# Kernel optimization log

Measured on AMD Instinct MI355X. Metric: run time of the kernel, lower is better.

Reference implementation:

```python
import jax, jax.numpy as jnp
import numpy as np

N_POL = 20000; N_COMP = 80000; N = N_POL + N_COMP
E = 1000000; EMB = 128; HID = 256; HEADS = 8; OUT = 128; EA = 5
NEG_SLOPE = 0.2; LN_EPS = 1e-5


def setup_inputs() -> dict:
    ks = jax.random.split(jax.random.key(0), 24)
    def rn(i, shape, s=0.1):
        return jax.random.normal(ks[i], shape, jnp.float32) * s
    C1 = HID // HEADS  # per-head channels of conv1
    return dict(
        pol_feat=rn(0, (N_POL, 7), 1.0),
        state_ids=jax.random.randint(ks[1], (N_POL,), 0, 55),
        comp_cat=jax.random.randint(ks[2], (N_COMP, 2), 0, 16),
        comp_price=rn(3, (N_COMP, 1), 1.0),
        edge_index=jax.random.randint(ks[4], (2, E), 0, N),
        edge_attr=rn(5, (E, EA), 1.0),
        Wp=rn(6, (7, EMB)), bp=jnp.zeros((EMB,), jnp.float32),
        state_emb=rn(7, (55, EMB)), sector_emb=rn(8, (16, 8)), industry_emb=rn(9, (150, 8)),
        Wc=rn(10, (17, EMB)), bc=jnp.zeros((EMB,), jnp.float32),
        ln_g=jnp.ones((EMB,), jnp.float32), ln_b=jnp.zeros((EMB,), jnp.float32),
        W1=rn(11, (EMB, HEADS * C1)), att_src1=rn(12, (HEADS, C1)), att_dst1=rn(13, (HEADS, C1)),
        We1=rn(14, (EA, HEADS * C1)), att_e1=rn(15, (HEADS, C1)), b1=jnp.zeros((HID,), jnp.float32),
        W2=rn(16, (HID, OUT)), att_src2=rn(17, (1, OUT)), att_dst2=rn(18, (1, OUT)),
        We2=rn(19, (EA, OUT)), att_e2=rn(20, (1, OUT)), b2=jnp.zeros((OUT,), jnp.float32),
    )


def _add_self_loops(src, dst, ea, n):
    # PyG add_self_loops with fill_value='mean': self-loop edge_attr = mean of
    # incoming edge attrs per dst node (0 for isolated nodes).
    loop = jnp.arange(n, dtype=src.dtype)
    cnt = jax.ops.segment_sum(jnp.ones(dst.shape, jnp.float32), dst, num_segments=n)
    loop_attr = jax.ops.segment_sum(ea, dst, num_segments=n) / jnp.maximum(cnt, 1.0)[:, None]
    return (jnp.concatenate([src, loop]), jnp.concatenate([dst, loop]),
            jnp.concatenate([ea, loop_attr], 0))


def _gat(x, src, dst, ea, W, a_src, a_dst, We, a_e, bias, concat):
    # PyG GATConv (shared lin for src/dst, edge_dim attention, eval mode).
    n = x.shape[0]
    H, C = a_src.shape
    xw = (x @ W).reshape(n, H, C)                 # [n,H,C]
    al_s = jnp.sum(xw * a_src, -1)                # [n,H]
    al_d = jnp.sum(xw * a_dst, -1)                # [n,H]
    ew = (ea @ We).reshape(-1, H, C)              # [Etot,H,C]
    al_e = jnp.sum(ew * a_e, -1)                  # [Etot,H]
    alpha = jax.nn.leaky_relu(al_s[src] + al_d[dst] + al_e, NEG_SLOPE)
    amax = jax.ops.segment_max(alpha, dst, num_segments=n)
    ex = jnp.exp(alpha - amax[dst])
    denom = jax.ops.segment_sum(ex, dst, num_segments=n)
    alpha = ex / (denom[dst] + 1e-16)             # segment softmax over dst
    out = jax.ops.segment_sum(xw[src] * alpha[:, :, None], dst, num_segments=n)
    out = out.reshape(n, H * C) if concat else out.mean(1)
    return out + bias


def reference(pol_feat, state_ids, comp_cat, comp_price, edge_index, edge_attr,
              Wp, bp, state_emb, sector_emb, industry_emb, Wc, bc, ln_g, ln_b,
              W1, att_src1, att_dst1, We1, att_e1, b1,
              W2, att_src2, att_dst2, We2, att_e2, b2):
    pol = jax.nn.relu(pol_feat @ Wp + bp) + state_emb[state_ids]
    comp_in = jnp.concatenate([sector_emb[comp_cat[:, 0]], industry_emb[comp_cat[:, 1]], comp_price], 1)
    comp = jax.nn.relu(comp_in @ Wc + bc)
    x = jnp.concatenate([pol, comp], 0)           # [N,EMB]
    mu = jnp.mean(x, -1, keepdims=True)
    var = jnp.var(x, -1, keepdims=True)
    x = (x - mu) / jnp.sqrt(var + LN_EPS) * ln_g + ln_b
    src, dst, ea = _add_self_loops(edge_index[0], edge_index[1], edge_attr, x.shape[0])
    h = jax.nn.elu(_gat(x, src, dst, ea, W1, att_src1, att_dst1, We1, att_e1, b1, True))
    return _gat(h, src, dst, ea, W2, att_src2, att_dst2, We2, att_e2, b2, False)
```

## Files before the change

kernel.cpp:

```cpp
#include <hip/hip_runtime.h>
#include <hip/hip_fp16.h>
#include <math.h>

#define N_POL 20000
#define N_COMP 80000
#define NN (N_POL + N_COMP)
#define EE 1000000
#define NB1 ((NN + 1023) / 1024)
#define LOG2E 1.44269504f

typedef short bf16x8 __attribute__((ext_vector_type(8)));
typedef float f32x4 __attribute__((ext_vector_type(4)));

struct __align__(16) PEdge {
  int s;
  float ale2;
  unsigned short a1[8];
  unsigned pad[2];
};

__device__ __forceinline__ float wave_sum(float v) {
#pragma unroll
  for (int o = 32; o > 0; o >>= 1) v += __shfl_xor(v, o);
  return v;
}
__device__ __forceinline__ float wave_max(float v) {
#pragma unroll
  for (int o = 32; o > 0; o >>= 1) v = fmaxf(v, __shfl_xor(v, o));
  return v;
}
__device__ __forceinline__ unsigned short f2bf(float f) {
  unsigned b = __float_as_uint(f);
  return (unsigned short)((b + 0x7FFFu + ((b >> 16) & 1u)) >> 16);
}
__device__ __forceinline__ float bf2f(unsigned short u) {
  return __uint_as_float(((unsigned)u) << 16);
}
__device__ __forceinline__ unsigned short f2h(float f) {
  __half h = __float2half_rn(f);
  return *(unsigned short*)&h;
}
__device__ __forceinline__ float h2f(unsigned short u) {
  __half h = *(__half*)&u;
  return __half2float(h);
}

__global__ __launch_bounds__(256) void k_prep(
    const float* W1, const float* W2, const float* as2, const float* ad2,
    const float* We1, const float* ae1, const float* We2, const float* ae2,
    const float* sector_emb, const float* industry_emb, const float* Wc,
    unsigned short* W1t, unsigned short* W2t, float* Ts, float* Ti, float* us2,
    float* ud2, float* V1, float* V2) {
  int id = blockIdx.x * 256 + threadIdx.x;
  if (id < 32768) {
    int n = id >> 7, k = id & 127;
    W1t[id] = f2bf(W1[k * 256 + n]);
  } else if (id < 65536) {
    int id2 = id - 32768;
    int n = id2 >> 8, k = id2 & 255;
    W2t[id2] = f2bf(W2[k * 128 + n]);
  } else if (id < 67584) {
    int id2 = id - 65536;
    int n = id2 >> 7, c = id2 & 127;
    float a = 0.f;
#pragma unroll
    for (int k = 0; k < 8; k++) a = fmaf(sector_emb[n * 8 + k], Wc[k * 128 + c], a);
    Ts[id2] = a;
  } else if (id < 86784) {
    int id2 = id - 67584;
    int n = id2 >> 7, c = id2 & 127;
    float a = 0.f;
#pragma unroll
    for (int k = 0; k < 8; k++) a = fmaf(industry_emb[n * 8 + k], Wc[(8 + k) * 128 + c], a);
    Ti[id2] = a;
  } else if (id < 87040) {
    int t = id - 86784;
    float s = 0.f, d = 0.f;
    for (int c = 0; c < 128; c++) {
      float w = W2[t * 128 + c];
      s = fmaf(w, as2[c], s);
      d = fmaf(w, ad2[c], d);
    }
    us2[t] = s * LOG2E;
    ud2[t] = d * LOG2E;
  } else if (id < 87104) {
    int t = id - 87040;
    int k = t >> 3, h = t & 7;
    if (k < 5) {
      float v = 0.f;
      for (int c = 0; c < 32; c++) v = fmaf(We1[k * 256 + h * 32 + c], ae1[h * 32 + c], v);
      V1[k * 8 + h] = v * LOG2E;
    }
  } else if (id < 87109) {
    int t = id - 87104;
    float v = 0.f;
    for (int c = 0; c < 128; c++) v = fmaf(We2[t * 128 + c], ae2[c], v);
    V2[t] = v * LOG2E;
  }
}

__global__ __launch_bounds__(256) void k_encode(
    const float* pol_feat, const int* state_ids, const int* comp_cat,
    const float* comp_price, const float* Wp, const float* bp, const float* state_emb,
    const float* Ts, const float* Ti, const float* Wc, const float* bc,
    const float* ln_g, const float* ln_b, unsigned short* x) {
  int t = threadIdx.x;
  int i = blockIdx.x * 2 + (t >> 7), c = t & 127;
  float v;
  if (i < N_POL) {
    float acc = bp[c];
#pragma unroll
    for (int k = 0; k < 7; k++) acc = fmaf(pol_feat[i * 7 + k], Wp[k * 128 + c], acc);
    v = fmaxf(acc, 0.f) + state_emb[state_ids[i] * 128 + c];
  } else {
    int j = i - N_POL;
    int sc = comp_cat[2 * j], in = comp_cat[2 * j + 1];
    float acc = Ts[sc * 128 + c] + Ti[in * 128 + c] +
                comp_price[j] * Wc[16 * 128 + c] + bc[c];
    v = fmaxf(acc, 0.f);
  }
  __shared__ float red[4];
  int wid = t >> 6, lane = t & 63;
  int base = (t >> 7) << 1;
  float s = wave_sum(v);
  if (lane == 0) red[wid] = s;
  __syncthreads();
  float mu = (red[base] + red[base + 1]) * (1.f / 128.f);
  float t0 = v - mu;
  __syncthreads();
  float s2 = wave_sum(t0 * t0);
  if (lane == 0) red[wid] = s2;
  __syncthreads();
  float var = (red[base] + red[base + 1]) * (1.f / 128.f);
  float r = rsqrtf(var + 1e-5f);
  float xf = t0 * r * ln_g[c] + ln_b[c];
  x[(size_t)i * 128 + c] = f2bf(xf);
}

__global__ void k_hist(const int* dst, unsigned* hist) {
  int e = blockIdx.x * blockDim.x + threadIdx.x;
  if (e < EE) atomicAdd(&hist[dst[e]], 1u);
}
__global__ __launch_bounds__(1024) void k_scan1(const unsigned* hist, unsigned* rowptr,
                                                unsigned* part) {
  __shared__ unsigned sc[1024];
  int t = threadIdx.x;
  int i = blockIdx.x * 1024 + t;
  unsigned v = (i < NN) ? hist[i] : 0u;
  sc[t] = v;
  __syncthreads();
  for (int o = 1; o < 1024; o <<= 1) {
    unsigned add = (t >= o) ? sc[t - o] : 0u;
    __syncthreads();
    sc[t] += add;
    __syncthreads();
  }
  if (i < NN) rowptr[i] = sc[t] - v;
  if (t == 1023) part[blockIdx.x] = sc[1023];
}
__global__ __launch_bounds__(128) void k_scan2(unsigned* part) {
  __shared__ unsigned sc[128];
  int t = threadIdx.x;
  unsigned v = (t < NB1) ? part[t] : 0u;
  sc[t] = v;
  __syncthreads();
  for (int o = 1; o < 128; o <<= 1) {
    unsigned add = (t >= o) ? sc[t - o] : 0u;
    __syncthreads();
    sc[t] += add;
    __syncthreads();
  }
  if (t < NB1) part[t] = sc[t] - v;
}
__global__ void k_scan3(unsigned* rowptr, const unsigned* part, unsigned* cursor) {
  int i = blockIdx.x * blockDim.x + threadIdx.x;
  if (i < NN) {
    unsigned r = rowptr[i] + part[i >> 10];
    rowptr[i] = r;
    cursor[i] = r;
  }
  if (i == 0) rowptr[NN] = EE;
}
__global__ void k_scatter(const int* src, const int* dst, const float* ea,
                          const float* V1, const float* V2, unsigned* cursor,
                          PEdge* ep) {
  int e = blockIdx.x * blockDim.x + threadIdx.x;
  if (e >= EE) return;
  int d = dst[e];
  unsigned pos = atomicAdd(&cursor[d], 1u);
  float av[5];
#pragma unroll
  for (int k = 0; k < 5; k++) av[k] = ea[(size_t)e * 5 + k];
  float a2 = 0.f;
#pragma unroll
  for (int k = 0; k < 5; k++) a2 = fmaf(av[k], V2[k], a2);
  unsigned short hb[8];
#pragma unroll
  for (int hh = 0; hh < 8; hh++) {
    float a1 = 0.f;
#pragma unroll
    for (int k = 0; k < 5; k++) a1 = fmaf(av[k], V1[k * 8 + hh], a1);
    hb[hh] = f2h(a1);
  }
  uint4 w0, w1;
  w0.x = (unsigned)src[e];
  w0.y = __float_as_uint(a2);
  w0.z = (unsigned)hb[0] | ((unsigned)hb[1] << 16);
  w0.w = (unsigned)hb[2] | ((unsigned)hb[3] << 16);
  w1.x = (unsigned)hb[4] | ((unsigned)hb[5] << 16);
  w1.y = (unsigned)hb[6] | ((unsigned)hb[7] << 16);
  w1.z = 0u; w1.w = 0u;
  uint4* p = (uint4*)(ep + pos);
  p[0] = w0;
  p[1] = w1;
}

__global__ __launch_bounds__(256) void k_gemm1(const unsigned short* x,
                                               const unsigned short* W1t,
                                               unsigned short* xw1) {
  __shared__ char wlds[65536];
  int tid = threadIdx.x;
#pragma unroll
  for (int it = 0; it < 16; it++) {
    int cch = it * 256 + tid;
    int row = cch >> 4, seg = cch & 15;
    uint4 v = *(const uint4*)(W1t + row * 128 + seg * 8);
    *(uint4*)(&wlds[(row * 256 + seg * 16) ^ ((row & 7) << 4)]) = v;
  }
  __syncthreads();
  int wid = tid >> 6, l = tid & 63;
  int cl = l & 15, kh = l >> 4;
  int swz = (cl & 7) << 4;
  long r0 = (long)blockIdx.x * 128 + wid * 32;
  f32x4 acc[2][16];
#pragma unroll
  for (int rt = 0; rt < 2; rt++)
#pragma unroll
    for (int nt = 0; nt < 16; nt++) acc[rt][nt] = {0.f, 0.f, 0.f, 0.f};
  long ra0 = r0 + cl; if (ra0 > NN - 1) ra0 = NN - 1;
  long ra1 = r0 + 16 + cl; if (ra1 > NN - 1) ra1 = NN - 1;
#pragma unroll
  for (int kk = 0; kk < 4; kk++) {
    bf16x8 a0 = *(const bf16x8*)(x + ra0 * 128 + kk * 32 + kh * 8);
    bf16x8 a1 = *(const bf16x8*)(x + ra1 * 128 + kk * 32 + kh * 8);
#pragma unroll
    for (int nt = 0; nt < 16; nt++) {
      bf16x8 b = *(const bf16x8*)(&wlds[(((nt * 16 + cl) * 256) + kk * 64 + kh * 16) ^ swz]);
      acc[0][nt] = __builtin_amdgcn_mfma_f32_16x16x32_bf16(a0, b, acc[0][nt], 0, 0, 0);
      acc[1][nt] = __builtin_amdgcn_mfma_f32_16x16x32_bf16(a1, b, acc[1][nt], 0, 0, 0);
    }
  }
#pragma unroll
  for (int rt = 0; rt < 2; rt++)
#pragma unroll
    for (int nt = 0; nt < 16; nt++)
#pragma unroll
      for (int j = 0; j < 4; j++) {
        long row = r0 + rt * 16 + kh * 4 + j;
        if (row < NN) xw1[row * 256 + nt * 16 + cl] = f2bf(acc[rt][nt][j]);
      }
}

__global__ __launch_bounds__(256) void k_al(const unsigned short* xw1, const float* as1,
                                            const float* ad1, float* al_s1,
                                            float* al_d1) {
  int w = threadIdx.x >> 6, lane = threadIdx.x & 63;
  int i = blockIdx.x * 4 + w;
  if (i >= NN) return;
  ushort4 xv = ((const ushort4*)(xw1 + (size_t)i * 256))[lane];
  float4 as = ((const float4*)as1)[lane];
  float4 ad = ((const float4*)ad1)[lane];
  float x0 = bf2f(xv.x), x1 = bf2f(xv.y), x2 = bf2f(xv.z), x3 = bf2f(xv.w);
  float s = x0 * as.x + x1 * as.y + x2 * as.z + x3 * as.w;
  float d = x0 * ad.x + x1 * ad.y + x2 * ad.z + x3 * ad.w;
#pragma unroll
  for (int o = 1; o < 8; o <<= 1) {
    s += __shfl_xor(s, o);
    d += __shfl_xor(d, o);
  }
  if ((lane & 7) == 0) {
    al_s1[i * 8 + (lane >> 3)] = s * LOG2E;
    al_d1[i * 8 + (lane >> 3)] = d * LOG2E;
  }
}

__global__ __launch_bounds__(256) void k_gemm2(const unsigned short* h,
                                               const unsigned short* W2t,
                                               unsigned short* xw2) {
  __shared__ char wlds[65536];
  int tid = threadIdx.x;
#pragma unroll
  for (int it = 0; it < 16; it++) {
    int cch = it * 256 + tid;
    int row = cch >> 5, seg = cch & 31;
    uint4 v = *(const uint4*)(W2t + row * 256 + seg * 8);
    *(uint4*)(&wlds[(row * 512 + seg * 16) ^ ((row & 7) << 4)]) = v;
  }
  __syncthreads();
  int wid = tid >> 6, l = tid & 63;
  int cl = l & 15, kh = l >> 4;
  int swz = (cl & 7) << 4;
  long r0 = (long)blockIdx.x * 128 + wid * 32;
  f32x4 acc[2][8];
#pragma unroll
  for (int rt = 0; rt < 2; rt++)
#pragma unroll
    for (int nt = 0; nt < 8; nt++) acc[rt][nt] = {0.f, 0.f, 0.f, 0.f};
  long ra0 = r0 + cl; if (ra0 > NN - 1) ra0 = NN - 1;
  long ra1 = r0 + 16 + cl; if (ra1 > NN - 1) ra1 = NN - 1;
#pragma unroll
  for (int kk = 0; kk < 8; kk++) {
    bf16x8 a0 = *(const bf16x8*)(h + ra0 * 256 + kk * 32 + kh * 8);
    bf16x8 a1 = *(const bf16x8*)(h + ra1 * 256 + kk * 32 + kh * 8);
#pragma unroll
    for (int nt = 0; nt < 8; nt++) {
      bf16x8 b = *(const bf16x8*)(&wlds[(((nt * 16 + cl) * 512) + kk * 64 + kh * 16) ^ swz]);
      acc[0][nt] = __builtin_amdgcn_mfma_f32_16x16x32_bf16(a0, b, acc[0][nt], 0, 0, 0);
      acc[1][nt] = __builtin_amdgcn_mfma_f32_16x16x32_bf16(a1, b, acc[1][nt], 0, 0, 0);
    }
  }
#pragma unroll
  for (int rt = 0; rt < 2; rt++)
#pragma unroll
    for (int nt = 0; nt < 8; nt++)
#pragma unroll
      for (int j = 0; j < 4; j++) {
        long row = r0 + rt * 16 + kh * 4 + j;
        if (row < NN) xw2[row * 128 + nt * 16 + cl] = f2bf(acc[rt][nt][j]);
      }
}

__global__ __launch_bounds__(256) void k_gat1(
    const unsigned* rowptr, const PEdge* ep, const float* al_s1, const float* al_d1,
    const unsigned short* xw1, const float* b1, const float* us2, const float* ud2,
    unsigned short* h, float* al_s2, float* al_d2) {
  int w = threadIdx.x >> 6, lane = threadIdx.x & 63;
  int i = blockIdx.x * 4 + w;
  if (i >= NN) return;
  int r0 = rowptr[i], r1 = rowptr[i + 1];
  int hh = lane & 7;
  int js = lane >> 3;
  int ah = lane >> 3;
  float ald = al_d1[i * 8 + hh];
  float m = -1e30f, l = 0.f;
  float a0 = 0.f, a1 = 0.f, a2 = 0.f, a3 = 0.f;
  float alesum = 0.f;

  auto chunk16 = [&](int jb) {
    int jc0 = jb + js, jc1 = jb + 8 + js;
    int s0 = *(const int*)&ep[jc0];
    int s1 = *(const int*)&ep[jc1];
    float e0 = h2f(((const unsigned short*)&ep[jc0])[4 + hh]);
    float e1 = h2f(((const unsigned short*)&ep[jc1])[4 + hh]);
    alesum += e0 + e1;
    float g0 = al_s1[s0 * 8 + hh] + ald + e0;
    g0 = g0 > 0.f ? g0 : 0.2f * g0;
    float g1 = al_s1[s1 * 8 + hh] + ald + e1;
    g1 = g1 > 0.f ? g1 : 0.2f * g1;
    float cm = fmaxf(g0, g1);
    cm = fmaxf(cm, __shfl_xor(cm, 8));
    cm = fmaxf(cm, __shfl_xor(cm, 16));
    cm = fmaxf(cm, __shfl_xor(cm, 32));
    float mn = fmaxf(m, cm);
    float sc = exp2f(m - mn);
    float p0 = exp2f(g0 - mn), p1 = exp2f(g1 - mn);
    float ps = p0 + p1;
    ps += __shfl_xor(ps, 8);
    ps += __shfl_xor(ps, 16);
    ps += __shfl_xor(ps, 32);
    l = l * sc + ps;
    m = mn;
    float asc = __shfl(sc, ah);
    a0 *= asc; a1 *= asc; a2 *= asc; a3 *= asc;
#pragma unroll
    for (int jj = 0; jj < 8; jj++) {
      float pj = __shfl(p0, jj * 8 + ah);
      int sj = __shfl(s0, jj * 8);
      ushort4 xv = ((const ushort4*)(xw1 + (size_t)sj * 256))[lane];
      a0 = fmaf(pj, bf2f(xv.x), a0);
      a1 = fmaf(pj, bf2f(xv.y), a1);
      a2 = fmaf(pj, bf2f(xv.z), a2);
      a3 = fmaf(pj, bf2f(xv.w), a3);
    }
#pragma unroll
    for (int jj = 0; jj < 8; jj++) {
      float pj = __shfl(p1, jj * 8 + ah);
      int sj = __shfl(s1, jj * 8);
      ushort4 xv = ((const ushort4*)(xw1 + (size_t)sj * 256))[lane];
      a0 = fmaf(pj, bf2f(xv.x), a0);
      a1 = fmaf(pj, bf2f(xv.y), a1);
      a2 = fmaf(pj, bf2f(xv.z), a2);
      a3 = fmaf(pj, bf2f(xv.w), a3);
    }
  };

  auto chunk8 = [&](int jb, int cnt) {
    bool valid = js < cnt;
    int jc = jb + (valid ? js : cnt - 1);
    int s = *(const int*)&ep[jc];
    float ale = h2f(((const unsigned short*)&ep[jc])[4 + hh]);
    if (!valid) ale = 0.f;
    alesum += ale;
    float logit = -1e30f;
    if (valid) {
      float al = al_s1[s * 8 + hh] + ald + ale;
      logit = al > 0.f ? al : 0.2f * al;
    }
    float cm = logit;
    cm = fmaxf(cm, __shfl_xor(cm, 8));
    cm = fmaxf(cm, __shfl_xor(cm, 16));
    cm = fmaxf(cm, __shfl_xor(cm, 32));
    float mn = fmaxf(m, cm);
    float sc = exp2f(m - mn);
    float p = exp2f(logit - mn);
    float ps = p;
    ps += __shfl_xor(ps, 8);
    ps += __shfl_xor(ps, 16);
    ps += __shfl_xor(ps, 32);
    l = l * sc + ps;
    m = mn;
    float asc = __shfl(sc, ah);
    a0 *= asc; a1 *= asc; a2 *= asc; a3 *= asc;
    for (int jj = 0; jj < cnt; jj++) {
      float pj = __shfl(p, jj * 8 + ah);
      int sj = __shfl(s, jj * 8);
      ushort4 xv = ((const ushort4*)(xw1 + (size_t)sj * 256))[lane];
      a0 = fmaf(pj, bf2f(xv.x), a0);
      a1 = fmaf(pj, bf2f(xv.y), a1);
      a2 = fmaf(pj, bf2f(xv.z), a2);
      a3 = fmaf(pj, bf2f(xv.w), a3);
    }
  };

  int jb = r0;
  for (; jb + 16 <= r1; jb += 16) chunk16(jb);
  if (jb + 8 <= r1) { chunk8(jb, 8); jb += 8; }
  if (jb < r1) chunk8(jb, r1 - jb);

  alesum += __shfl_xor(alesum, 8);
  alesum += __shfl_xor(alesum, 16);
  alesum += __shfl_xor(alesum, 32);
  float inv = 1.f / fmaxf((float)(r1 - r0), 1.f);
  float aleS = alesum * inv;
  {
    float al = al_s1[i * 8 + hh] + ald + aleS;
    float logit = al > 0.f ? al : 0.2f * al;
    float mn = fmaxf(m, logit);
    float sc = exp2f(m - mn);
    float p = exp2f(logit - mn);
    l = l * sc + p;
    m = mn;
    float asc = __shfl(sc, ah);
    float pj = __shfl(p, ah);
    ushort4 xv = ((const ushort4*)(xw1 + (size_t)i * 256))[lane];
    a0 = fmaf(pj, bf2f(xv.x), a0 * asc);
    a1 = fmaf(pj, bf2f(xv.y), a1 * asc);
    a2 = fmaf(pj, bf2f(xv.z), a2 * asc);
    a3 = fmaf(pj, bf2f(xv.w), a3 * asc);
  }
  float lh = __shfl(l, ah);
  float invl = 1.f / (lh + 1e-16f);
  float4 bv = ((const float4*)b1)[lane];
  float v0 = a0 * invl + bv.x, v1 = a1 * invl + bv.y;
  float v2 = a2 * invl + bv.z, v3 = a3 * invl + bv.w;
  v0 = v0 > 0.f ? v0 : expm1f(v0);
  v1 = v1 > 0.f ? v1 : expm1f(v1);
  v2 = v2 > 0.f ? v2 : expm1f(v2);
  v3 = v3 > 0.f ? v3 : expm1f(v3);
  ushort4 hv;
  hv.x = f2bf(v0); hv.y = f2bf(v1); hv.z = f2bf(v2); hv.w = f2bf(v3);
  ((ushort4*)(h + (size_t)i * 256))[lane] = hv;
  float4 uv = ((const float4*)us2)[lane];
  float4 dv = ((const float4*)ud2)[lane];
  float ps2 = v0 * uv.x + v1 * uv.y + v2 * uv.z + v3 * uv.w;
  float pd2 = v0 * dv.x + v1 * dv.y + v2 * dv.z + v3 * dv.w;
  ps2 = wave_sum(ps2);
  pd2 = wave_sum(pd2);
  if (lane == 0) { al_s2[i] = ps2; al_d2[i] = pd2; }
}

__global__ __launch_bounds__(256) void k_gat2(
    const unsigned* rowptr, const PEdge* ep, const float* al_s2, const float* al_d2,
    const unsigned short* xw2, const float* b2, float* out) {
  int w = threadIdx.x >> 6, lane = threadIdx.x & 63;
  int i = blockIdx.x * 4 + w;
  if (i >= NN) return;
  int r0 = rowptr[i], r1 = rowptr[i + 1];
  float ald = al_d2[i];
  float m = -1e30f, l = 0.f, a0 = 0.f, a1 = 0.f;
  float alesum = 0.f;

  auto chunk = [&](int jb, int cnt) {
    bool valid = lane < cnt;
    int jc = jb + (valid ? lane : cnt - 1);
    int2 sv = *(const int2*)&ep[jc];
    int s = sv.x;
    float ale = valid ? __uint_as_float((unsigned)sv.y) : 0.f;
    alesum += ale;
    float logit = -1e30f;
    if (valid) {
      float al = al_s2[s] + ald + ale;
      logit = al > 0.f ? al : 0.2f * al;
    }
    float cm = wave_max(logit);
    float mn = fmaxf(m, cm);
    float sc = exp2f(m - mn);
    float p = exp2f(logit - mn);
    float ps = wave_sum(p);
    l = l * sc + ps;
    m = mn;
    a0 *= sc; a1 *= sc;
    for (int jj = 0; jj < cnt; jj++) {
      float pj = __shfl(p, jj);
      int sj = __shfl(s, jj);
      ushort2 xv = ((const ushort2*)(xw2 + (size_t)sj * 128))[lane];
      a0 = fmaf(pj, bf2f(xv.x), a0);
      a1 = fmaf(pj, bf2f(xv.y), a1);
    }
  };
  int jb = r0;
  for (; jb + 64 <= r1; jb += 64) chunk(jb, 64);
  if (jb < r1) chunk(jb, r1 - jb);

  alesum = wave_sum(alesum);
  float inv = 1.f / fmaxf((float)(r1 - r0), 1.f);
  float aleS = alesum * inv;
  {
    float al = al_s2[i] + ald + aleS;
    float logit = al > 0.f ? al : 0.2f * al;
    float mn = fmaxf(m, logit);
    float sc = exp2f(m - mn);
    float p = exp2f(logit - mn);
    l = l * sc + p;
    ushort2 xv = ((const ushort2*)(xw2 + (size_t)i * 128))[lane];
    a0 = fmaf(p, bf2f(xv.x), a0 * sc);
    a1 = fmaf(p, bf2f(xv.y), a1 * sc);
  }
  float invl = 1.f / (l + 1e-16f);
  float2 bv = ((const float2*)b2)[lane];
  float2 ov = {a0 * invl + bv.x, a1 * invl + bv.y};
  ((float2*)(out + (size_t)i * 128))[lane] = ov;
}

extern "C" void kernel_launch(void* const* d_in, const int* in_sizes, int n_in,
                              void* d_out, int out_size, void* d_ws, size_t ws_size,
                              hipStream_t stream) {
  const float* pol_feat = (const float*)d_in[0];
  const int* state_ids = (const int*)d_in[1];
  const int* comp_cat = (const int*)d_in[2];
  const float* comp_price = (const float*)d_in[3];
  const int* edge_index = (const int*)d_in[4];
  const float* edge_attr = (const float*)d_in[5];
  const float* Wp = (const float*)d_in[6];
  const float* bp = (const float*)d_in[7];
  const float* state_emb = (const float*)d_in[8];
  const float* sector_emb = (const float*)d_in[9];
  const float* industry_emb = (const float*)d_in[10];
  const float* Wc = (const float*)d_in[11];
  const float* bc = (const float*)d_in[12];
  const float* ln_g = (const float*)d_in[13];
  const float* ln_b = (const float*)d_in[14];
  const float* W1 = (const float*)d_in[15];
  const float* as1 = (const float*)d_in[16];
  const float* ad1 = (const float*)d_in[17];
  const float* We1 = (const float*)d_in[18];
  const float* ae1 = (const float*)d_in[19];
  const float* b1 = (const float*)d_in[20];
  const float* W2 = (const float*)d_in[21];
  const float* as2 = (const float*)d_in[22];
  const float* ad2 = (const float*)d_in[23];
  const float* We2 = (const float*)d_in[24];
  const float* ae2 = (const float*)d_in[25];
  const float* b2 = (const float*)d_in[26];
  const int* srcv = edge_index;
  const int* dstv = edge_index + EE;
  float* out = (float*)d_out;

  size_t off = 0;
  auto alloc = [&](size_t nbytes) -> char* {
    char* p = (char*)d_ws + off;
    off += ((nbytes + 255) & ~(size_t)255);
    return p;
  };
  char* regA = alloc((size_t)NN * 512);
  char* regB = alloc((size_t)NN * 512);
  unsigned short* xw1 = (unsigned short*)regA;
  unsigned short* xw2 = (unsigned short*)regA;
  unsigned short* h = (unsigned short*)regB;
  unsigned short* x = (unsigned short*)regB;
  float* al_s1 = (float*)alloc((size_t)NN * 8 * 4);
  float* al_d1 = (float*)alloc((size_t)NN * 8 * 4);
  float* al_s2 = (float*)alloc((size_t)NN * 4);
  float* al_d2 = (float*)alloc((size_t)NN * 4);
  float* us2 = (float*)alloc(256 * 4);
  float* ud2 = (float*)alloc(256 * 4);
  float* V1 = (float*)alloc(64 * 4);
  float* V2 = (float*)alloc(8 * 4);
  float* Ts = (float*)alloc(16 * 128 * 4);
  float* Ti = (float*)alloc(150 * 128 * 4);
  unsigned short* W1t = (unsigned short*)alloc(32768 * 2);
  unsigned short* W2t = (unsigned short*)alloc(32768 * 2);
  unsigned* hist = (unsigned*)alloc((size_t)NN * 4);
  unsigned* rowptr = (unsigned*)alloc((size_t)(NN + 1) * 4);
  unsigned* cursor = (unsigned*)alloc((size_t)NN * 4);
  unsigned* part = (unsigned*)alloc((size_t)NB1 * 4);
  PEdge* ep = (PEdge*)alloc((size_t)EE * sizeof(PEdge));

  hipMemsetAsync(hist, 0, (size_t)NN * 4, stream);

  k_prep<<<341, 256, 0, stream>>>(W1, W2, as2, ad2, We1, ae1, We2, ae2, sector_emb,
                                  industry_emb, Wc, W1t, W2t, Ts, Ti, us2, ud2, V1, V2);
  k_encode<<<NN / 2, 256, 0, stream>>>(pol_feat, state_ids, comp_cat, comp_price, Wp,
                                       bp, state_emb, Ts, Ti, Wc, bc, ln_g, ln_b, x);
  k_hist<<<(EE + 255) / 256, 256, 0, stream>>>(dstv, hist);
  k_scan1<<<NB1, 1024, 0, stream>>>(hist, rowptr, part);
  k_scan2<<<1, 128, 0, stream>>>(part);
  k_scan3<<<(NN + 255) / 256, 256, 0, stream>>>(rowptr, part, cursor);
  k_scatter<<<(EE + 255) / 256, 256, 0, stream>>>(srcv, dstv, edge_attr, V1, V2,
                                                  cursor, ep);
  k_gemm1<<<(NN + 127) / 128, 256, 0, stream>>>(x, W1t, xw1);
  k_al<<<NN / 4, 256, 0, stream>>>(xw1, as1, ad1, al_s1, al_d1);
  k_gat1<<<NN / 4, 256, 0, stream>>>(rowptr, ep, al_s1, al_d1, xw1, b1, us2, ud2, h,
                                     al_s2, al_d2);
  k_gemm2<<<(NN + 127) / 128, 256, 0, stream>>>(h, W2t, xw2);
  k_gat2<<<NN / 4, 256, 0, stream>>>(rowptr, ep, al_s2, al_d2, xw2, b2, out);
}
```

Measured before the change: 420.9 us.

## Shrink edge records to raw fp16 attrs, fuse attention logits into gemm1

Each edge record shrinks from 32 to 16 bytes. It now holds the source index and the five raw edge attributes in fp16, and the per-head edge logits are recomputed inside the GAT kernels from V1/V2. The attention-source/destination dot products move into the gemm1 epilogue via lane shuffles, which removes the separate k_al pass over xw1. The scan2 kernel is folded into scan3, so every block redoes the 128-entry prefix, and gat2 gains a fully populated 64-edge chunk path. The aim is less memory traffic and fewer launches, paid for with more ALU work per edge and a small change in fp16 rounding of the edge logits.

```diff
diff --git a/kernel.cpp b/kernel.cpp
--- a/kernel.cpp
+++ b/kernel.cpp
@@ -12,12 +12,6 @@
 typedef short bf16x8 __attribute__((ext_vector_type(8)));
 typedef float f32x4 __attribute__((ext_vector_type(4)));
 
-struct __align__(16) PEdge {
-  int s;
-  float ale2;
-  unsigned short a1[8];
-  unsigned pad[2];
-};
 
 __device__ __forceinline__ float wave_sum(float v) {
 #pragma unroll
@@ -40,9 +34,9 @@
   __half h = __float2half_rn(f);
   return *(unsigned short*)&h;
 }
-__device__ __forceinline__ float h2f(unsigned short u) {
-  __half h = *(__half*)&u;
-  return __half2float(h);
+__device__ __forceinline__ float2 h2f2(unsigned u) {
+  __half2 h = *(__half2*)&u;
+  return __half22float2(h);
 }
 
 __global__ __launch_bounds__(256) void k_prep(
@@ -158,32 +152,35 @@
   if (i < NN) rowptr[i] = sc[t] - v;
   if (t == 1023) part[blockIdx.x] = sc[1023];
 }
-__global__ __launch_bounds__(128) void k_scan2(unsigned* part) {
-  __shared__ unsigned sc[128];
+__global__ __launch_bounds__(256) void k_scan3(unsigned* rowptr, const unsigned* part,
+                                               unsigned* cursor) {
+  __shared__ unsigned pref[128];
   int t = threadIdx.x;
-  unsigned v = (t < NB1) ? part[t] : 0u;
-  sc[t] = v;
+  unsigned orig = 0u;
+  if (t < 128) {
+    orig = (t < NB1) ? part[t] : 0u;
+    pref[t] = orig;
+  }
   __syncthreads();
   for (int o = 1; o < 128; o <<= 1) {
-    unsigned add = (t >= o) ? sc[t - o] : 0u;
+    unsigned add = 0u;
+    if (t < 128 && t >= o) add = pref[t - o];
     __syncthreads();
-    sc[t] += add;
+    if (t < 128) pref[t] += add;
     __syncthreads();
   }
-  if (t < NB1) part[t] = sc[t] - v;
-}
-__global__ void k_scan3(unsigned* rowptr, const unsigned* part, unsigned* cursor) {
-  int i = blockIdx.x * blockDim.x + threadIdx.x;
+  if (t < 128) pref[t] -= orig;
+  __syncthreads();
+  int i = blockIdx.x * 256 + t;
   if (i < NN) {
-    unsigned r = rowptr[i] + part[i >> 10];
+    unsigned r = rowptr[i] + pref[i >> 10];
     rowptr[i] = r;
     cursor[i] = r;
   }
   if (i == 0) rowptr[NN] = EE;
 }
 __global__ void k_scatter(const int* src, const int* dst, const float* ea,
-                          const float* V1, const float* V2, unsigned* cursor,
-                          PEdge* ep) {
+                          unsigned* cursor, uint4* ep) {
   int e = blockIdx.x * blockDim.x + threadIdx.x;
   if (e >= EE) return;
   int d = dst[e];
@@ -191,33 +188,19 @@
   float av[5];
 #pragma unroll
   for (int k = 0; k < 5; k++) av[k] = ea[(size_t)e * 5 + k];
-  float a2 = 0.f;
-#pragma unroll
-  for (int k = 0; k < 5; k++) a2 = fmaf(av[k], V2[k], a2);
-  unsigned short hb[8];
-#pragma unroll
-  for (int hh = 0; hh < 8; hh++) {
-    float a1 = 0.f;
-#pragma unroll
-    for (int k = 0; k < 5; k++) a1 = fmaf(av[k], V1[k * 8 + hh], a1);
-    hb[hh] = f2h(a1);
-  }
-  uint4 w0, w1;
-  w0.x = (unsigned)src[e];
-  w0.y = __float_as_uint(a2);
-  w0.z = (unsigned)hb[0] | ((unsigned)hb[1] << 16);
-  w0.w = (unsigned)hb[2] | ((unsigned)hb[3] << 16);
-  w1.x = (unsigned)hb[4] | ((unsigned)hb[5] << 16);
-  w1.y = (unsigned)hb[6] | ((unsigned)hb[7] << 16);
-  w1.z = 0u; w1.w = 0u;
-  uint4* p = (uint4*)(ep + pos);
-  p[0] = w0;
-  p[1] = w1;
+  uint4 w;
+  w.x = (unsigned)src[e];
+  w.y = (unsigned)f2h(av[0]) | ((unsigned)f2h(av[1]) << 16);
+  w.z = (unsigned)f2h(av[2]) | ((unsigned)f2h(av[3]) << 16);
+  w.w = (unsigned)f2h(av[4]);
+  ep[pos] = w;
 }
 
 __global__ __launch_bounds__(256) void k_gemm1(const unsigned short* x,
                                                const unsigned short* W1t,
-                                               unsigned short* xw1) {
+                                               const float* as1, const float* ad1,
+                                               unsigned short* xw1, float* al_s1,
+                                               float* al_d1) {
   __shared__ char wlds[65536];
   int tid = threadIdx.x;
 #pragma unroll
@@ -250,38 +233,38 @@
       acc[1][nt] = __builtin_amdgcn_mfma_f32_16x16x32_bf16(a1, b, acc[1][nt], 0, 0, 0);
     }
   }
+  float as1s[16], ad1s[16];
+#pragma unroll
+  for (int nt = 0; nt < 16; nt++) {
+    as1s[nt] = as1[nt * 16 + cl];
+    ad1s[nt] = ad1[nt * 16 + cl];
+  }
 #pragma unroll
   for (int rt = 0; rt < 2; rt++)
 #pragma unroll
-    for (int nt = 0; nt < 16; nt++)
-#pragma unroll
-      for (int j = 0; j < 4; j++) {
-        long row = r0 + rt * 16 + kh * 4 + j;
-        if (row < NN) xw1[row * 256 + nt * 16 + cl] = f2bf(acc[rt][nt][j]);
+    for (int j = 0; j < 4; j++) {
+      long row = r0 + rt * 16 + kh * 4 + j;
+      bool ok = row < NN;
+#pragma unroll
+      for (int hh = 0; hh < 8; hh++) {
+        float a0 = acc[rt][2 * hh][j];
+        float a1 = acc[rt][2 * hh + 1][j];
+        if (ok) {
+          xw1[row * 256 + (2 * hh) * 16 + cl] = f2bf(a0);
+          xw1[row * 256 + (2 * hh + 1) * 16 + cl] = f2bf(a1);
+        }
+        float sh = a0 * as1s[2 * hh] + a1 * as1s[2 * hh + 1];
+        float dh = a0 * ad1s[2 * hh] + a1 * ad1s[2 * hh + 1];
+        sh += __shfl_xor(sh, 1); sh += __shfl_xor(sh, 2);
+        sh += __shfl_xor(sh, 4); sh += __shfl_xor(sh, 8);
+        dh += __shfl_xor(dh, 1); dh += __shfl_xor(dh, 2);
+        dh += __shfl_xor(dh, 4); dh += __shfl_xor(dh, 8);
+        if (ok && cl == 0) {
+          al_s1[row * 8 + hh] = sh * LOG2E;
+          al_d1[row * 8 + hh] = dh * LOG2E;
+        }
       }
-}
-
-__global__ __launch_bounds__(256) void k_al(const unsigned short* xw1, const float* as1,
-                                            const float* ad1, float* al_s1,
-                                            float* al_d1) {
-  int w = threadIdx.x >> 6, lane = threadIdx.x & 63;
-  int i = blockIdx.x * 4 + w;
-  if (i >= NN) return;
-  ushort4 xv = ((const ushort4*)(xw1 + (size_t)i * 256))[lane];
-  float4 as = ((const float4*)as1)[lane];
-  float4 ad = ((const float4*)ad1)[lane];
-  float x0 = bf2f(xv.x), x1 = bf2f(xv.y), x2 = bf2f(xv.z), x3 = bf2f(xv.w);
-  float s = x0 * as.x + x1 * as.y + x2 * as.z + x3 * as.w;
-  float d = x0 * ad.x + x1 * ad.y + x2 * ad.z + x3 * ad.w;
-#pragma unroll
-  for (int o = 1; o < 8; o <<= 1) {
-    s += __shfl_xor(s, o);
-    d += __shfl_xor(d, o);
-  }
-  if ((lane & 7) == 0) {
-    al_s1[i * 8 + (lane >> 3)] = s * LOG2E;
-    al_d1[i * 8 + (lane >> 3)] = d * LOG2E;
-  }
+    }
 }
 
 __global__ __launch_bounds__(256) void k_gemm2(const unsigned short* h,
@@ -331,9 +314,9 @@
 }
 
 __global__ __launch_bounds__(256) void k_gat1(
-    const unsigned* rowptr, const PEdge* ep, const float* al_s1, const float* al_d1,
-    const unsigned short* xw1, const float* b1, const float* us2, const float* ud2,
-    unsigned short* h, float* al_s2, float* al_d2) {
+    const unsigned* rowptr, const uint4* ep, const float* al_s1, const float* al_d1,
+    const float* V1, const unsigned short* xw1, const float* b1, const float* us2,
+    const float* ud2, unsigned short* h, float* al_s2, float* al_d2) {
   int w = threadIdx.x >> 6, lane = threadIdx.x & 63;
   int i = blockIdx.x * 4 + w;
   if (i >= NN) return;
@@ -341,17 +324,25 @@
   int hh = lane & 7;
   int js = lane >> 3;
   int ah = lane >> 3;
+  float v1k0 = V1[0 * 8 + hh], v1k1 = V1[1 * 8 + hh], v1k2 = V1[2 * 8 + hh];
+  float v1k3 = V1[3 * 8 + hh], v1k4 = V1[4 * 8 + hh];
   float ald = al_d1[i * 8 + hh];
   float m = -1e30f, l = 0.f;
   float a0 = 0.f, a1 = 0.f, a2 = 0.f, a3 = 0.f;
   float alesum = 0.f;
 
+  auto edot = [&](const uint4& rec) {
+    float2 e01 = h2f2(rec.y);
+    float2 e23 = h2f2(rec.z);
+    float e4 = h2f2(rec.w).x;
+    return e01.x * v1k0 + e01.y * v1k1 + e23.x * v1k2 + e23.y * v1k3 + e4 * v1k4;
+  };
+
   auto chunk16 = [&](int jb) {
-    int jc0 = jb + js, jc1 = jb + 8 + js;
-    int s0 = *(const int*)&ep[jc0];
-    int s1 = *(const int*)&ep[jc1];
-    float e0 = h2f(((const unsigned short*)&ep[jc0])[4 + hh]);
-    float e1 = h2f(((const unsigned short*)&ep[jc1])[4 + hh]);
+    uint4 rc0 = ep[jb + js];
+    uint4 rc1 = ep[jb + 8 + js];
+    int s0 = (int)rc0.x, s1 = (int)rc1.x;
+    float e0 = edot(rc0), e1 = edot(rc1);
     alesum += e0 + e1;
     float g0 = al_s1[s0 * 8 + hh] + ald + e0;
     g0 = g0 > 0.f ? g0 : 0.2f * g0;
@@ -397,8 +388,9 @@
   auto chunk8 = [&](int jb, int cnt) {
     bool valid = js < cnt;
     int jc = jb + (valid ? js : cnt - 1);
-    int s = *(const int*)&ep[jc];
-    float ale = h2f(((const unsigned short*)&ep[jc])[4 + hh]);
+    uint4 rc = ep[jc];
+    int s = (int)rc.x;
+    float ale = edot(rc);
     if (!valid) ale = 0.f;
     alesum += ale;
     float logit = -1e30f;
@@ -480,22 +472,56 @@
 }
 
 __global__ __launch_bounds__(256) void k_gat2(
-    const unsigned* rowptr, const PEdge* ep, const float* al_s2, const float* al_d2,
-    const unsigned short* xw2, const float* b2, float* out) {
+    const unsigned* rowptr, const uint4* ep, const float* al_s2, const float* al_d2,
+    const float* V2, const unsigned short* xw2, const float* b2, float* out) {
   int w = threadIdx.x >> 6, lane = threadIdx.x & 63;
   int i = blockIdx.x * 4 + w;
   if (i >= NN) return;
   int r0 = rowptr[i], r1 = rowptr[i + 1];
+  float v2k0 = V2[0], v2k1 = V2[1], v2k2 = V2[2], v2k3 = V2[3], v2k4 = V2[4];
   float ald = al_d2[i];
   float m = -1e30f, l = 0.f, a0 = 0.f, a1 = 0.f;
   float alesum = 0.f;
 
+  auto edot = [&](const uint4& rec) {
+    float2 e01 = h2f2(rec.y);
+    float2 e23 = h2f2(rec.z);
+    float e4 = h2f2(rec.w).x;
+    return e01.x * v2k0 + e01.y * v2k1 + e23.x * v2k2 + e23.y * v2k3 + e4 * v2k4;
+  };
+
+  auto chunkF = [&](int jb) {
+    uint4 rc = ep[jb + lane];
+    int s = (int)rc.x;
+    float ale = edot(rc);
+    alesum += ale;
+    float al = al_s2[s] + ald + ale;
+    float logit = al > 0.f ? al : 0.2f * al;
+    float cm = wave_max(logit);
+    float mn = fmaxf(m, cm);
+    float sc = exp2f(m - mn);
+    float p = exp2f(logit - mn);
+    float ps = wave_sum(p);
+    l = l * sc + ps;
+    m = mn;
+    a0 *= sc; a1 *= sc;
+#pragma unroll 4
+    for (int jj = 0; jj < 64; jj++) {
+      float pj = __shfl(p, jj);
+      int sj = __shfl(s, jj);
+      ushort2 xv = ((const ushort2*)(xw2 + (size_t)sj * 128))[lane];
+      a0 = fmaf(pj, bf2f(xv.x), a0);
+      a1 = fmaf(pj, bf2f(xv.y), a1);
+    }
+  };
+
   auto chunk = [&](int jb, int cnt) {
     bool valid = lane < cnt;
     int jc = jb + (valid ? lane : cnt - 1);
-    int2 sv = *(const int2*)&ep[jc];
-    int s = sv.x;
-    float ale = valid ? __uint_as_float((unsigned)sv.y) : 0.f;
+    uint4 rc = ep[jc];
+    int s = (int)rc.x;
+    float ale = edot(rc);
+    if (!valid) ale = 0.f;
     alesum += ale;
     float logit = -1e30f;
     if (valid) {
@@ -518,8 +544,9 @@
       a1 = fmaf(pj, bf2f(xv.y), a1);
     }
   };
+
   int jb = r0;
-  for (; jb + 64 <= r1; jb += 64) chunk(jb, 64);
+  for (; jb + 64 <= r1; jb += 64) chunkF(jb);
   if (jb < r1) chunk(jb, r1 - jb);
 
   alesum = wave_sum(alesum);
@@ -604,7 +631,7 @@
   unsigned* rowptr = (unsigned*)alloc((size_t)(NN + 1) * 4);
   unsigned* cursor = (unsigned*)alloc((size_t)NN * 4);
   unsigned* part = (unsigned*)alloc((size_t)NB1 * 4);
-  PEdge* ep = (PEdge*)alloc((size_t)EE * sizeof(PEdge));
+  uint4* ep = (uint4*)alloc((size_t)EE * 16);
 
   hipMemsetAsync(hist, 0, (size_t)NN * 4, stream);
 
@@ -614,14 +641,11 @@
                                        bp, state_emb, Ts, Ti, Wc, bc, ln_g, ln_b, x);
   k_hist<<<(EE + 255) / 256, 256, 0, stream>>>(dstv, hist);
   k_scan1<<<NB1, 1024, 0, stream>>>(hist, rowptr, part);
-  k_scan2<<<1, 128, 0, stream>>>(part);
   k_scan3<<<(NN + 255) / 256, 256, 0, stream>>>(rowptr, part, cursor);
-  k_scatter<<<(EE + 255) / 256, 256, 0, stream>>>(srcv, dstv, edge_attr, V1, V2,
-                                                  cursor, ep);
-  k_gemm1<<<(NN + 127) / 128, 256, 0, stream>>>(x, W1t, xw1);
-  k_al<<<NN / 4, 256, 0, stream>>>(xw1, as1, ad1, al_s1, al_d1);
-  k_gat1<<<NN / 4, 256, 0, stream>>>(rowptr, ep, al_s1, al_d1, xw1, b1, us2, ud2, h,
-                                     al_s2, al_d2);
+  k_scatter<<<(EE + 255) / 256, 256, 0, stream>>>(srcv, dstv, edge_attr, cursor, ep);
+  k_gemm1<<<(NN + 127) / 128, 256, 0, stream>>>(x, W1t, as1, ad1, xw1, al_s1, al_d1);
+  k_gat1<<<NN / 4, 256, 0, stream>>>(rowptr, ep, al_s1, al_d1, V1, xw1, b1, us2, ud2,
+                                     h, al_s2, al_d2);
   k_gemm2<<<(NN + 127) / 128, 256, 0, stream>>>(h, W2t, xw2);
-  k_gat2<<<NN / 4, 256, 0, stream>>>(rowptr, ep, al_s2, al_d2, xw2, b2, out);
-}
+  k_gat2<<<NN / 4, 256, 0, stream>>>(rowptr, ep, al_s2, al_d2, V2, xw2, b2, out);
+}
```

Result: slower. 452.5 us (+7.5%).

## Horizontally fuse hist into prep, scan2 into scan3, and scatter with GEMM1

Applied to the files above, without the earlier changes.

Merges independent kernels into shared launches. The histogram atomics ride as extra blocks of the prep kernel. The small part-scan is recomputed inside every scan3 block through shared memory. The edge scatter and the first MFMA GEMM are interleaved in one grid, with every sixth block doing GEMM work. This cuts kernel launches and the serialization gaps between them and lets the GEMM overlap the atomic-heavy scatter. The trade-off is that scatter blocks now carry the GEMM's 64KB static LDS allocation, which can sharply limit their occupancy.

```diff
diff --git a/kernel.cpp b/kernel.cpp
--- a/kernel.cpp
+++ b/kernel.cpp
@@ -8,6 +8,9 @@
 #define EE 1000000
 #define NB1 ((NN + 1023) / 1024)
 #define LOG2E 1.44269504f
+#define GB1 ((NN + 127) / 128)
+#define SB ((EE + 255) / 256)
+#define PB 341
 
 typedef short bf16x8 __attribute__((ext_vector_type(8)));
 typedef float f32x4 __attribute__((ext_vector_type(4)));
@@ -45,13 +48,19 @@
   return __half2float(h);
 }
 
-__global__ __launch_bounds__(256) void k_prep(
+__global__ __launch_bounds__(256) void k_fuse1(
     const float* W1, const float* W2, const float* as2, const float* ad2,
     const float* We1, const float* ae1, const float* We2, const float* ae2,
     const float* sector_emb, const float* industry_emb, const float* Wc,
-    unsigned short* W1t, unsigned short* W2t, float* Ts, float* Ti, float* us2,
-    float* ud2, float* V1, float* V2) {
-  int id = blockIdx.x * 256 + threadIdx.x;
+    const int* dst, unsigned short* W1t, unsigned short* W2t, float* Ts, float* Ti,
+    float* us2, float* ud2, float* V1, float* V2, unsigned* hist) {
+  int bid = blockIdx.x;
+  if (bid >= PB) {
+    int e = (bid - PB) * 256 + threadIdx.x;
+    if (e < EE) atomicAdd(&hist[dst[e]], 1u);
+    return;
+  }
+  int id = bid * 256 + threadIdx.x;
   if (id < 32768) {
     int n = id >> 7, k = id & 127;
     W1t[id] = f2bf(W1[k * 256 + n]);
@@ -137,10 +146,6 @@
   x[(size_t)i * 128 + c] = f2bf(xf);
 }
 
-__global__ void k_hist(const int* dst, unsigned* hist) {
-  int e = blockIdx.x * blockDim.x + threadIdx.x;
-  if (e < EE) atomicAdd(&hist[dst[e]], 1u);
-}
 __global__ __launch_bounds__(1024) void k_scan1(const unsigned* hist, unsigned* rowptr,
                                                 unsigned* part) {
   __shared__ unsigned sc[1024];
@@ -158,107 +163,114 @@
   if (i < NN) rowptr[i] = sc[t] - v;
   if (t == 1023) part[blockIdx.x] = sc[1023];
 }
-__global__ __launch_bounds__(128) void k_scan2(unsigned* part) {
-  __shared__ unsigned sc[128];
+__global__ __launch_bounds__(256) void k_scan3(unsigned* rowptr, const unsigned* part,
+                                               unsigned* cursor) {
+  __shared__ unsigned pref[128];
   int t = threadIdx.x;
-  unsigned v = (t < NB1) ? part[t] : 0u;
-  sc[t] = v;
+  unsigned orig = 0u;
+  if (t < 128) {
+    orig = (t < NB1) ? part[t] : 0u;
+    pref[t] = orig;
+  }
   __syncthreads();
   for (int o = 1; o < 128; o <<= 1) {
-    unsigned add = (t >= o) ? sc[t - o] : 0u;
+    unsigned add = 0u;
+    if (t < 128 && t >= o) add = pref[t - o];
     __syncthreads();
-    sc[t] += add;
+    if (t < 128) pref[t] += add;
     __syncthreads();
   }
-  if (t < NB1) part[t] = sc[t] - v;
-}
-__global__ void k_scan3(unsigned* rowptr, const unsigned* part, unsigned* cursor) {
-  int i = blockIdx.x * blockDim.x + threadIdx.x;
+  if (t < 128) pref[t] -= orig;
+  __syncthreads();
+  int i = blockIdx.x * 256 + t;
   if (i < NN) {
-    unsigned r = rowptr[i] + part[i >> 10];
+    unsigned r = rowptr[i] + pref[i >> 10];
     rowptr[i] = r;
     cursor[i] = r;
   }
   if (i == 0) rowptr[NN] = EE;
 }
-__global__ void k_scatter(const int* src, const int* dst, const float* ea,
-                          const float* V1, const float* V2, unsigned* cursor,
-                          PEdge* ep) {
-  int e = blockIdx.x * blockDim.x + threadIdx.x;
-  if (e >= EE) return;
-  int d = dst[e];
-  unsigned pos = atomicAdd(&cursor[d], 1u);
-  float av[5];
-#pragma unroll
-  for (int k = 0; k < 5; k++) av[k] = ea[(size_t)e * 5 + k];
-  float a2 = 0.f;
-#pragma unroll
-  for (int k = 0; k < 5; k++) a2 = fmaf(av[k], V2[k], a2);
-  unsigned short hb[8];
-#pragma unroll
-  for (int hh = 0; hh < 8; hh++) {
-    float a1 = 0.f;
-#pragma unroll
-    for (int k = 0; k < 5; k++) a1 = fmaf(av[k], V1[k * 8 + hh], a1);
-    hb[hh] = f2h(a1);
-  }
-  uint4 w0, w1;
-  w0.x = (unsigned)src[e];
-  w0.y = __float_as_uint(a2);
-  w0.z = (unsigned)hb[0] | ((unsigned)hb[1] << 16);
-  w0.w = (unsigned)hb[2] | ((unsigned)hb[3] << 16);
-  w1.x = (unsigned)hb[4] | ((unsigned)hb[5] << 16);
-  w1.y = (unsigned)hb[6] | ((unsigned)hb[7] << 16);
-  w1.z = 0u; w1.w = 0u;
-  uint4* p = (uint4*)(ep + pos);
-  p[0] = w0;
-  p[1] = w1;
-}
-
-__global__ __launch_bounds__(256) void k_gemm1(const unsigned short* x,
-                                               const unsigned short* W1t,
-                                               unsigned short* xw1) {
+
+__global__ __launch_bounds__(256) void k_fuse2(
+    const unsigned short* x, const unsigned short* W1t, unsigned short* xw1,
+    const int* src, const int* dst, const float* ea, const float* V1, const float* V2,
+    unsigned* cursor, PEdge* ep) {
   __shared__ char wlds[65536];
-  int tid = threadIdx.x;
-#pragma unroll
-  for (int it = 0; it < 16; it++) {
-    int cch = it * 256 + tid;
-    int row = cch >> 4, seg = cch & 15;
-    uint4 v = *(const uint4*)(W1t + row * 128 + seg * 8);
-    *(uint4*)(&wlds[(row * 256 + seg * 16) ^ ((row & 7) << 4)]) = v;
-  }
-  __syncthreads();
-  int wid = tid >> 6, l = tid & 63;
-  int cl = l & 15, kh = l >> 4;
-  int swz = (cl & 7) << 4;
-  long r0 = (long)blockIdx.x * 128 + wid * 32;
-  f32x4 acc[2][16];
-#pragma unroll
-  for (int rt = 0; rt < 2; rt++)
-#pragma unroll
-    for (int nt = 0; nt < 16; nt++) acc[rt][nt] = {0.f, 0.f, 0.f, 0.f};
-  long ra0 = r0 + cl; if (ra0 > NN - 1) ra0 = NN - 1;
-  long ra1 = r0 + 16 + cl; if (ra1 > NN - 1) ra1 = NN - 1;
-#pragma unroll
-  for (int kk = 0; kk < 4; kk++) {
-    bf16x8 a0 = *(const bf16x8*)(x + ra0 * 128 + kk * 32 + kh * 8);
-    bf16x8 a1 = *(const bf16x8*)(x + ra1 * 128 + kk * 32 + kh * 8);
-#pragma unroll
-    for (int nt = 0; nt < 16; nt++) {
-      bf16x8 b = *(const bf16x8*)(&wlds[(((nt * 16 + cl) * 256) + kk * 64 + kh * 16) ^ swz]);
-      acc[0][nt] = __builtin_amdgcn_mfma_f32_16x16x32_bf16(a0, b, acc[0][nt], 0, 0, 0);
-      acc[1][nt] = __builtin_amdgcn_mfma_f32_16x16x32_bf16(a1, b, acc[1][nt], 0, 0, 0);
-    }
-  }
-#pragma unroll
-  for (int rt = 0; rt < 2; rt++)
-#pragma unroll
-    for (int nt = 0; nt < 16; nt++)
-#pragma unroll
-      for (int j = 0; j < 4; j++) {
-        long row = r0 + rt * 16 + kh * 4 + j;
-        if (row < NN) xw1[row * 256 + nt * 16 + cl] = f2bf(acc[rt][nt][j]);
+  int bid = blockIdx.x;
+  if (bid % 6 == 0) {
+    int gb = bid / 6;
+    int tid = threadIdx.x;
+#pragma unroll
+    for (int it = 0; it < 16; it++) {
+      int cch = it * 256 + tid;
+      int row = cch >> 4, seg = cch & 15;
+      uint4 v = *(const uint4*)(W1t + row * 128 + seg * 8);
+      *(uint4*)(&wlds[(row * 256 + seg * 16) ^ ((row & 7) << 4)]) = v;
+    }
+    __syncthreads();
+    int wid = tid >> 6, l = tid & 63;
+    int cl = l & 15, kh = l >> 4;
+    int swz = (cl & 7) << 4;
+    long r0 = (long)gb * 128 + wid * 32;
+    f32x4 acc[2][16];
+#pragma unroll
+    for (int rt = 0; rt < 2; rt++)
+#pragma unroll
+      for (int nt = 0; nt < 16; nt++) acc[rt][nt] = {0.f, 0.f, 0.f, 0.f};
+    long ra0 = r0 + cl; if (ra0 > NN - 1) ra0 = NN - 1;
+    long ra1 = r0 + 16 + cl; if (ra1 > NN - 1) ra1 = NN - 1;
+#pragma unroll
+    for (int kk = 0; kk < 4; kk++) {
+      bf16x8 a0 = *(const bf16x8*)(x + ra0 * 128 + kk * 32 + kh * 8);
+      bf16x8 a1 = *(const bf16x8*)(x + ra1 * 128 + kk * 32 + kh * 8);
+#pragma unroll
+      for (int nt = 0; nt < 16; nt++) {
+        bf16x8 b = *(const bf16x8*)(&wlds[(((nt * 16 + cl) * 256) + kk * 64 + kh * 16) ^ swz]);
+        acc[0][nt] = __builtin_amdgcn_mfma_f32_16x16x32_bf16(a0, b, acc[0][nt], 0, 0, 0);
+        acc[1][nt] = __builtin_amdgcn_mfma_f32_16x16x32_bf16(a1, b, acc[1][nt], 0, 0, 0);
       }
+    }
+#pragma unroll
+    for (int rt = 0; rt < 2; rt++)
+#pragma unroll
+      for (int nt = 0; nt < 16; nt++)
+#pragma unroll
+        for (int j = 0; j < 4; j++) {
+          long row = r0 + rt * 16 + kh * 4 + j;
+          if (row < NN) xw1[row * 256 + nt * 16 + cl] = f2bf(acc[rt][nt][j]);
+        }
+  } else {
+    int sidx = bid - bid / 6 - 1;
+    int e = sidx * 256 + threadIdx.x;
+    if (e >= EE) return;
+    int d = dst[e];
+    unsigned pos = atomicAdd(&cursor[d], 1u);
+    float av[5];
+#pragma unroll
+    for (int k = 0; k < 5; k++) av[k] = ea[(size_t)e * 5 + k];
+    float a2 = 0.f;
+#pragma unroll
+    for (int k = 0; k < 5; k++) a2 = fmaf(av[k], V2[k], a2);
+    unsigned short hb[8];
+#pragma unroll
+    for (int hh = 0; hh < 8; hh++) {
+      float a1 = 0.f;
+#pragma unroll
+      for (int k = 0; k < 5; k++) a1 = fmaf(av[k], V1[k * 8 + hh], a1);
+      hb[hh] = f2h(a1);
+    }
+    uint4 w0, w1;
+    w0.x = (unsigned)src[e];
+    w0.y = __float_as_uint(a2);
+    w0.z = (unsigned)hb[0] | ((unsigned)hb[1] << 16);
+    w0.w = (unsigned)hb[2] | ((unsigned)hb[3] << 16);
+    w1.x = (unsigned)hb[4] | ((unsigned)hb[5] << 16);
+    w1.y = (unsigned)hb[6] | ((unsigned)hb[7] << 16);
+    w1.z = 0u; w1.w = 0u;
+    uint4* p = (uint4*)(ep + pos);
+    p[0] = w0;
+    p[1] = w1;
+  }
 }
 
 __global__ __launch_bounds__(256) void k_al(const unsigned short* xw1, const float* as1,
@@ -348,8 +360,8 @@
 
   auto chunk16 = [&](int jb) {
     int jc0 = jb + js, jc1 = jb + 8 + js;
-    int s0 = *(const int*)&ep[jc0];
-    int s1 = *(const int*)&ep[jc1];
+    int s0 = ((const int*)&ep[jc0])[0];
+    int s1 = ((const int*)&ep[jc1])[0];
     float e0 = h2f(((const unsigned short*)&ep[jc0])[4 + hh]);
     float e1 = h2f(((const unsigned short*)&ep[jc1])[4 + hh]);
     alesum += e0 + e1;
@@ -397,7 +409,7 @@
   auto chunk8 = [&](int jb, int cnt) {
     bool valid = js < cnt;
     int jc = jb + (valid ? js : cnt - 1);
-    int s = *(const int*)&ep[jc];
+    int s = ((const int*)&ep[jc])[0];
     float ale = h2f(((const unsigned short*)&ep[jc])[4 + hh]);
     if (!valid) ale = 0.f;
     alesum += ale;
@@ -608,17 +620,15 @@
 
   hipMemsetAsync(hist, 0, (size_t)NN * 4, stream);
 
-  k_prep<<<341, 256, 0, stream>>>(W1, W2, as2, ad2, We1, ae1, We2, ae2, sector_emb,
-                                  industry_emb, Wc, W1t, W2t, Ts, Ti, us2, ud2, V1, V2);
+  k_fuse1<<<PB + SB, 256, 0, stream>>>(W1, W2, as2, ad2, We1, ae1, We2, ae2,
+                                       sector_emb, industry_emb, Wc, dstv, W1t, W2t,
+                                       Ts, Ti, us2, ud2, V1, V2, hist);
   k_encode<<<NN / 2, 256, 0, stream>>>(pol_feat, state_ids, comp_cat, comp_price, Wp,
                                        bp, state_emb, Ts, Ti, Wc, bc, ln_g, ln_b, x);
-  k_hist<<<(EE + 255) / 256, 256, 0, stream>>>(dstv, hist);
   k_scan1<<<NB1, 1024, 0, stream>>>(hist, rowptr, part);
-  k_scan2<<<1, 128, 0, stream>>>(part);
   k_scan3<<<(NN + 255) / 256, 256, 0, stream>>>(rowptr, part, cursor);
-  k_scatter<<<(EE + 255) / 256, 256, 0, stream>>>(srcv, dstv, edge_attr, V1, V2,
-                                                  cursor, ep);
-  k_gemm1<<<(NN + 127) / 128, 256, 0, stream>>>(x, W1t, xw1);
+  k_fuse2<<<GB1 * 6 + (SB - GB1 * 5), 256, 0, stream>>>(x, W1t, xw1, srcv, dstv,
+                                                        edge_attr, V1, V2, cursor, ep);
   k_al<<<NN / 4, 256, 0, stream>>>(xw1, as1, ad1, al_s1, al_d1);
   k_gat1<<<NN / 4, 256, 0, stream>>>(rowptr, ep, al_s1, al_d1, xw1, b1, us2, ud2, h,
                                      al_s2, al_d2);
```

Result: faster. 403.0 us (-4.3%).
